# Kernel optimization log

Hardware: AMD Instinct MI355X
Metric: run time of the kernel (lower is better)

The kernel has to match this reference:

```python
import jax, jax.numpy as jnp
import numpy as np

R_SPHERE = 3.0   # bounding_sphere_radius
NEAR = 0.0       # near_distance
FAR = 100.0      # far_distance
SECANT_STEPS = 4 # manifold_secant_steps
EPS = 1e-4
R0 = 1.0         # base radius of analytic manifold field


def setup_inputs() -> dict:
    key = jax.random.key(0)
    ks = jax.random.split(key, 6)
    B, R, L, H = 4, 8192, 4, 64
    rays_o = jax.random.normal(ks[0], (B, R, 3), dtype=jnp.float32) * 0.2  # origins inside sphere
    rd = jax.random.normal(ks[1], (B, R, 3), dtype=jnp.float32)
    rays_d = rd / jnp.linalg.norm(rd, axis=-1, keepdims=True)
    levels = jnp.linspace(0.5, -0.5, L, dtype=jnp.float32)  # manifold_levels parameter
    W1 = jax.random.normal(ks[2], (3, H), dtype=jnp.float32) * 0.3
    b1 = jnp.zeros((H,), dtype=jnp.float32)
    W2 = jax.random.normal(ks[3], (H, 1), dtype=jnp.float32) * 0.1
    b2 = jnp.zeros((1,), dtype=jnp.float32)
    rays_idx = jax.random.randint(ks[4], (B, R), 0, B, dtype=jnp.int64) if jax.config.jax_enable_x64 else jax.random.randint(ks[4], (B, R), 0, B, dtype=jnp.int32)
    mask_gt = jnp.ones((B, R), dtype=bool)
    return {"rays_o": rays_o, "rays_d": rays_d, "levels": levels, "W1": W1, "b1": b1,
            "W2": W2, "b2": b2, "mask_gt": mask_gt, "rays_idx": rays_idx, "num_samples": 64}


def _ray_march(rays_o, rays_d, levels, W1, b1, W2, b2, num_samples):
    B, Rn = rays_o.shape[:2]
    N = B * Rn
    L = levels.shape[0]
    o = rays_o.reshape(N, 3)
    d = rays_d.reshape(N, 3)

    def manifold_fn(x):
        # analytic stand-in for M(x_d, idx): scalar field + validity mask
        h = jnp.tanh(x @ W1 + b1)
        nrm = jnp.linalg.norm(x, axis=-1)
        s = (h @ W2)[..., 0] + b2[0] + (R0 - nrm)
        return s, nrm < R_SPHERE

    # ray-sphere intersection (unit-norm directions assumed, as in source)
    b = jnp.sum(o * d, axis=-1)
    c = jnp.sum(o * o, axis=-1) - R_SPHERE ** 2
    disc = b * b - c
    hit = disc > 0
    sq = jnp.sqrt(jnp.where(hit, disc, 1.0))
    d_near = jnp.maximum(-b - sq, NEAR)
    d_far = jnp.minimum(-b + sq, FAR)
    mask_bound = hit & (d_near < d_far)

    # stratified (uniform) depth samples, (N, S)
    t = jnp.linspace(0.0, 1.0, num_samples, dtype=rays_o.dtype)[None, :]
    ds = d_near[:, None] * (1 - t) + d_far[:, None] * t
    x_d = o[:, None, :] + d[:, None, :] * ds[..., None]  # (N, S, 3)
    scal, m_valid = manifold_fn(x_d)                      # (N, S)

    # --- find_closest_interval ---
    S = num_samples
    dep_f, dep_b = ds[:, :-1], ds[:, 1:]
    sc_f, sc_b = scal[:, :-1], scal[:, 1:]
    m_pair = m_valid[:, :-1] & m_valid[:, 1:]
    l3 = levels[None, :, None]                            # (1, L, 1)
    in_interval = (sc_f[:, None, :] >= l3) & (l3 >= sc_b[:, None, :]) & m_pair[:, None, :]
    rank = jnp.sign(l3 - sc_b[:, None, :]) * jnp.arange(S - 1, 0, -1, dtype=scal.dtype)
    ind_closest = jnp.argmax(rank, axis=2)                # (N, L)
    ind_lowest = jnp.broadcast_to(jnp.argmin(sc_b, axis=1)[:, None], (N, L))
    mask_surface = jnp.any(in_interval, axis=2)
    idx = jnp.where(mask_surface, ind_closest, ind_lowest)
    d_front = jnp.take_along_axis(dep_f, idx, axis=1)
    d_back = jnp.take_along_axis(dep_b, idx, axis=1)
    s_front = jnp.take_along_axis(sc_f, idx, axis=1)
    s_back = jnp.take_along_axis(sc_b, idx, axis=1)

    # --- find_exact_intersection ---
    lr = levels[None, :]                                  # (1, L)
    s_diff = s_front - s_back
    m_vdiff = jnp.abs(s_diff) > EPS
    mask_intersect = (s_front >= lr) & (lr >= s_back)
    mask_secant = mask_intersect & m_vdiff
    s_diff_safe = jnp.where(m_vdiff, s_diff, 1.0)
    d_secant = ((lr - s_back) * d_front + (s_front - lr) * d_back) / s_diff_safe
    d_init = jnp.where(mask_secant, d_secant, d_back)

    # secant refinement (fixed step count; masked full-array updates replace
    # torch's boolean-indexed subset updates with identical math on masked lanes)
    dfs, dbs, sfs, sbs, dcur = d_front, d_back, s_front, s_back, d_init
    for _ in range(SECANT_STEPS):
        x_mid = o[:, None, :] + dcur[..., None] * d[:, None, :]  # (N, L, 3)
        s_mid, mv = manifold_fn(x_mid)
        upf = (s_mid > lr) & mv
        upb = (s_mid < lr) & mv
        dfs = jnp.where(upf, dcur, dfs)
        sfs = jnp.where(upf, s_mid, sfs)
        dbs = jnp.where(upb, dcur, dbs)
        sbs = jnp.where(upb, s_mid, sbs)
        sd = sfs - sbs
        ok = jnp.abs(sd) > EPS
        dcur = jnp.where(ok, ((lr - sbs) * dfs + (sfs - lr) * dbs) / jnp.where(ok, sd, 1.0), dcur)
    d_intersect = jnp.where(mask_secant, dcur, d_init)

    # sort intersections by depth (use_presort=False branch)
    order = jnp.argsort(d_intersect, axis=1)
    d_intersect = jnp.take_along_axis(d_intersect, order, axis=1)
    mask_intersect = jnp.take_along_axis(mask_intersect, order, axis=1)

    dist = jnp.where(mask_bound[:, None], d_intersect, 0.0).reshape(B, Rn, L)
    mask = (mask_intersect & mask_bound[:, None]).reshape(B, Rn, L)
    return dist, mask


def reference(rays_o, rays_d, levels, W1, b1, W2, b2, mask_gt, rays_idx, num_samples):
    # mask_gt / rays_idx are unused in eval mode (use_gt_mask_when_training=False,
    # analytic manifold_fn ignores batch index), kept for signature fidelity.
    return _ray_march(rays_o, rays_d, levels, W1, b1, W2, b2, num_samples)
```

## Files before the change

kernel.cpp:

```cpp
#include <hip/hip_runtime.h>
#include <cstdint>

#define R_SPHEREf 3.0f
#define NEARf 0.0f
#define FARf 100.0f
#define SECANT_STEPS 4
#define EPSf 1e-4f
#define R0f 1.0f
#define Hh 64
#define Lc 4
#define Sn 64

#define C_HI 2.88539004325866699f
#define C_LO 3.8519227871e-08f

__global__ __launch_bounds__(256) void manifold_render_kernel(
    const float* __restrict__ rays_o, const float* __restrict__ rays_d,
    const float* __restrict__ levels, const float* __restrict__ W1,
    const float* __restrict__ b1, const float* __restrict__ W2,
    const float* __restrict__ b2, float* __restrict__ out, int N)
{
    __shared__ float4 abq[4][Hh];

    const int tid = threadIdx.x;
    const int wave = tid >> 6;
    const int lane = tid & 63;
    const int r = blockIdx.x * 4 + wave;
    const bool ray_ok = (r < N);

    const float b2v = b2[0];
    float lvl[Lc];
#pragma unroll
    for (int j = 0; j < Lc; ++j) lvl[j] = levels[j];

    float ox = 0.f, oy = 0.f, oz = 0.f, dx = 0.f, dy = 0.f, dz = 1.f;
    if (ray_ok) {
        ox = rays_o[3 * r]; oy = rays_o[3 * r + 1]; oz = rays_o[3 * r + 2];
        dx = rays_d[3 * r]; dy = rays_d[3 * r + 1]; dz = rays_d[3 * r + 2];
    }

    float w2lane;
    {
        const float w1x = W1[lane], w1y = W1[Hh + lane], w1z = W1[2 * Hh + lane];
        w2lane = W2[lane];
        const float Ah = __builtin_fmaf(oz, w1z, __builtin_fmaf(oy, w1y,
                         __builtin_fmaf(ox, w1x, b1[lane])));
        const float Bh = __builtin_fmaf(dz, w1z, __builtin_fmaf(dy, w1y, dx * w1x));
        const float A2 = __builtin_fmaf(Ah, C_LO, Ah * C_HI);
        const float B2 = __builtin_fmaf(Bh, C_LO, Bh * C_HI);
        abq[wave][lane] = make_float4(A2, B2, -2.0f * w2lane, 0.0f);
    }
    float w2sum = w2lane;
#pragma unroll
    for (int m = 1; m < 64; m <<= 1) w2sum += __shfl_xor(w2sum, m);
    const float sbase = w2sum + b2v + R0f;

    __syncthreads();
    if (!ray_ok) return;

    const float bq = ox * dx + oy * dy + oz * dz;
    const float cq = ox * ox + oy * oy + oz * oz - R_SPHEREf * R_SPHEREf;
    const float disc = bq * bq - cq;
    const bool hit = disc > 0.0f;
    const float sq = sqrtf(hit ? disc : 1.0f);
    const float d_near = fmaxf(-bq - sq, NEARf);
    const float d_far  = fminf(-bq + sq, FARf);
    const bool mask_bound = hit && (d_near < d_far);

    const float t = (float)lane / (float)(Sn - 1);
    const float dsv = d_near * (1.0f - t) + d_far * t;
    const float x0 = ox + dx * dsv, x1 = oy + dy * dsv, x2 = oz + dz * dsv;
    const float nrm = sqrtf(x0 * x0 + x1 * x1 + x2 * x2);

    const float4* __restrict__ ab = &abq[wave][0];
    float acc = 0.0f;
#pragma unroll
    for (int h = 0; h < Hh; ++h) {
        const float4 q = ab[h];
        const float y = __builtin_fmaf(dsv, q.y, q.x);
        const float e = __builtin_amdgcn_exp2f(y);
        const float r1 = __builtin_amdgcn_rcpf(e + 1.0f);
        acc = __builtin_fmaf(q.z, r1, acc);
    }
    const float scal = (acc + sbase) - nrm;
    const bool valid = nrm < R_SPHEREf;

    const float scb = __shfl_down(scal, 1);
    const int validn = __shfl_down((int)valid, 1);
    const bool is_int = lane < (Sn - 1);

    float keyv = is_int ? scb : INFINITY;
    int keyi = lane;
#pragma unroll
    for (int m = 1; m < 64; m <<= 1) {
        float ov = __shfl_xor(keyv, m);
        int oi = __shfl_xor(keyi, m);
        if (ov < keyv || (ov == keyv && oi < keyi)) { keyv = ov; keyi = oi; }
    }
    const int ind_lowest = keyi;

    const bool inint_base = is_int && valid && (validn != 0);

    bool mintb[Lc], msec[Lc];
    float dinit[Lc];
    float g_dfs = 0.f, g_dbs = 0.f, g_sfs = 0.f, g_sbs = 0.f, g_dcur = 0.f, g_lr = 0.f;
    const int g = lane >> 4;

#pragma unroll
    for (int lv = 0; lv < Lc; ++lv) {
        const float l = lvl[lv];
        unsigned long long bP = __ballot(is_int && (scb < l));
        unsigned long long bZ = __ballot(is_int && (scb == l));
        unsigned long long bI = __ballot(inint_base && (scal >= l) && (l >= scb));
        int ind_closest = bP ? __builtin_ctzll(bP)
                             : (bZ ? __builtin_ctzll(bZ) : (Sn - 2));
        bool mask_surface = (bI != 0ULL);
        int idx = mask_surface ? ind_closest : ind_lowest;

        float d_front = __shfl(dsv, idx);
        float d_back  = __shfl(dsv, idx + 1);
        float s_front = __shfl(scal, idx);
        float s_back  = __shfl(scal, idx + 1);

        bool mi = (s_front >= l) && (l >= s_back);
        float sd = s_front - s_back;
        bool vd = fabsf(sd) > EPSf;
        bool ms = mi && vd;
        float d_sec = ((l - s_back) * d_front + (s_front - l) * d_back) / (vd ? sd : 1.0f);
        float di = ms ? d_sec : d_back;

        mintb[lv] = mi; msec[lv] = ms; dinit[lv] = di;
        if (g == lv) {
            g_dfs = d_front; g_dbs = d_back; g_sfs = s_front; g_sbs = s_back;
            g_dcur = di; g_lr = l;
        }
    }

    const int sub = lane & 15;
    float4 sq0 = ab[sub], sq1 = ab[sub + 16], sq2 = ab[sub + 32], sq3 = ab[sub + 48];

#pragma unroll
    for (int it = 0; it < SECANT_STEPS; ++it) {
        float mx0 = ox + g_dcur * dx, mx1 = oy + g_dcur * dy, mx2 = oz + g_dcur * dz;
        float mn = sqrtf(mx0 * mx0 + mx1 * mx1 + mx2 * mx2);
        float part;
        {
            float y0 = __builtin_fmaf(g_dcur, sq0.y, sq0.x);
            float y1 = __builtin_fmaf(g_dcur, sq1.y, sq1.x);
            float y2 = __builtin_fmaf(g_dcur, sq2.y, sq2.x);
            float y3 = __builtin_fmaf(g_dcur, sq3.y, sq3.x);
            float r0 = __builtin_amdgcn_rcpf(__builtin_amdgcn_exp2f(y0) + 1.0f);
            float r1 = __builtin_amdgcn_rcpf(__builtin_amdgcn_exp2f(y1) + 1.0f);
            float r2 = __builtin_amdgcn_rcpf(__builtin_amdgcn_exp2f(y2) + 1.0f);
            float r3 = __builtin_amdgcn_rcpf(__builtin_amdgcn_exp2f(y3) + 1.0f);
            part = sq0.z * r0;
            part = __builtin_fmaf(sq1.z, r1, part);
            part = __builtin_fmaf(sq2.z, r2, part);
            part = __builtin_fmaf(sq3.z, r3, part);
        }
#pragma unroll
        for (int m = 1; m < 16; m <<= 1) part += __shfl_xor(part, m, 16);
        float s_mid = (part + sbase) - mn;
        bool mv = mn < R_SPHEREf;
        bool upf = (s_mid > g_lr) && mv;
        bool upb = (s_mid < g_lr) && mv;
        if (upf) { g_dfs = g_dcur; g_sfs = s_mid; }
        if (upb) { g_dbs = g_dcur; g_sbs = s_mid; }
        float sd2 = g_sfs - g_sbs;
        bool ok = fabsf(sd2) > EPSf;
        if (ok) g_dcur = ((g_lr - g_sbs) * g_dfs + (g_sfs - g_lr) * g_dbs) / sd2;
    }

    float v0, v1, v2, v3;
    {
        float dc0 = __shfl(g_dcur, 0);
        float dc1 = __shfl(g_dcur, 16);
        float dc2 = __shfl(g_dcur, 32);
        float dc3 = __shfl(g_dcur, 48);
        v0 = msec[0] ? dc0 : dinit[0];
        v1 = msec[1] ? dc1 : dinit[1];
        v2 = msec[2] ? dc2 : dinit[2];
        v3 = msec[3] ? dc3 : dinit[3];
    }
    int m0 = mintb[0], m1 = mintb[1], m2 = mintb[2], m3 = mintb[3];
    int i0 = 0, i1 = 1, i2 = 2, i3 = 3;

#define CSWAP(va, ia, ma, vb, ib, mb)                                    \
    { bool sw = (vb < va) || (vb == va && ib < ia);                      \
      if (sw) { float tv = va; va = vb; vb = tv;                         \
                int ti = ia; ia = ib; ib = ti;                           \
                int tm = ma; ma = mb; mb = tm; } }
    CSWAP(v0, i0, m0, v1, i1, m1);
    CSWAP(v2, i2, m2, v3, i3, m3);
    CSWAP(v0, i0, m0, v2, i2, m2);
    CSWAP(v1, i1, m1, v3, i3, m3);
    CSWAP(v1, i1, m1, v2, i2, m2);
#undef CSWAP

    const long long NL = (long long)N * Lc;
    if (lane < Lc) {
        float dv = (lane == 0) ? v0 : (lane == 1) ? v1 : (lane == 2) ? v2 : v3;
        out[(long long)r * Lc + lane] = mask_bound ? dv : 0.0f;
    } else if (lane < 2 * Lc) {
        int k = lane - Lc;
        int mm = (k == 0) ? m0 : (k == 1) ? m1 : (k == 2) ? m2 : m3;
        out[NL + (long long)r * Lc + k] = (mm && mask_bound) ? 1.0f : 0.0f;
    }
}

extern "C" void kernel_launch(void* const* d_in, const int* in_sizes, int n_in,
                              void* d_out, int out_size, void* d_ws, size_t ws_size,
                              hipStream_t stream) {
    const float* rays_o = (const float*)d_in[0];
    const float* rays_d = (const float*)d_in[1];
    const float* levels = (const float*)d_in[2];
    const float* W1 = (const float*)d_in[3];
    const float* b1 = (const float*)d_in[4];
    const float* W2 = (const float*)d_in[5];
    const float* b2 = (const float*)d_in[6];
    float* out = (float*)d_out;

    const int N = in_sizes[0] / 3;
    const int blocks = (N + 3) / 4;
    manifold_render_kernel<<<blocks, 256, 0, stream>>>(
        rays_o, rays_d, levels, W1, b1, W2, b2, out, N);
}
```

Before: 130.3 us.

## Use DPP row rotations instead of LDS broadcasts and shuffles in MLP loop

The hidden-unit loop no longer reads each of the 64 coefficient float4s from LDS. Each lane loads four float4s and rotates them across its 16-lane row with DPP row_ror, so the whole row covers all units without LDS traffic. The first four butterfly steps of the argmin and the 16-lane secant reduction also switch from ds_swizzle/bpermute shuffles to DPP row rotations. This trades LDS reads for three extra VALU DPP moves per hidden unit and changes the summation order of the field values.

```diff
diff --git a/kernel.cpp b/kernel.cpp
--- a/kernel.cpp
+++ b/kernel.cpp
@@ -13,6 +13,24 @@
 
 #define C_HI 2.88539004325866699f
 #define C_LO 3.8519227871e-08f
+
+template <int CTRL>
+__device__ __forceinline__ float dpp_rot(float v) {
+    int i = __float_as_int(v);
+    int r = __builtin_amdgcn_update_dpp(i, i, CTRL, 0xF, 0xF, false);
+    return __int_as_float(r);
+}
+template <int CTRL>
+__device__ __forceinline__ int dpp_rot_i(int v) {
+    return __builtin_amdgcn_update_dpp(v, v, CTRL, 0xF, 0xF, false);
+}
+__device__ __forceinline__ float row16_sum(float x) {
+    x += dpp_rot<0x128>(x);
+    x += dpp_rot<0x124>(x);
+    x += dpp_rot<0x122>(x);
+    x += dpp_rot<0x121>(x);
+    return x;
+}
 
 __global__ __launch_bounds__(256) void manifold_render_kernel(
     const float* __restrict__ rays_o, const float* __restrict__ rays_d,
@@ -73,14 +91,29 @@
     const float nrm = sqrtf(x0 * x0 + x1 * x1 + x2 * x2);
 
     const float4* __restrict__ ab = &abq[wave][0];
+    const int Rrow = lane >> 4;
+    const int s16 = lane & 15;
+
+    float4 qq[4];
+#pragma unroll
+    for (int k = 0; k < 4; ++k) qq[k] = ab[(((Rrow + k) & 3) << 4) + s16];
+
     float acc = 0.0f;
 #pragma unroll
-    for (int h = 0; h < Hh; ++h) {
-        const float4 q = ab[h];
-        const float y = __builtin_fmaf(dsv, q.y, q.x);
-        const float e = __builtin_amdgcn_exp2f(y);
-        const float r1 = __builtin_amdgcn_rcpf(e + 1.0f);
-        acc = __builtin_fmaf(q.z, r1, acc);
+    for (int k = 0; k < 4; ++k) {
+        float cA = qq[k].x, cB = qq[k].y, cW = qq[k].z;
+#pragma unroll
+        for (int i = 0; i < 16; ++i) {
+            const float y = __builtin_fmaf(dsv, cB, cA);
+            const float e = __builtin_amdgcn_exp2f(y);
+            const float r1 = __builtin_amdgcn_rcpf(e + 1.0f);
+            acc = __builtin_fmaf(cW, r1, acc);
+            if (i < 15) {
+                cA = dpp_rot<0x121>(cA);
+                cB = dpp_rot<0x121>(cB);
+                cW = dpp_rot<0x121>(cW);
+            }
+        }
     }
     const float scal = (acc + sbase) - nrm;
     const bool valid = nrm < R_SPHEREf;
@@ -91,8 +124,16 @@
 
     float keyv = is_int ? scb : INFINITY;
     int keyi = lane;
-#pragma unroll
-    for (int m = 1; m < 64; m <<= 1) {
+#define ARGMIN_STEP_DPP(CTRL)                                            \
+    { float ov = dpp_rot<CTRL>(keyv); int oi = dpp_rot_i<CTRL>(keyi);    \
+      if (ov < keyv || (ov == keyv && oi < keyi)) { keyv = ov; keyi = oi; } }
+    ARGMIN_STEP_DPP(0x128)
+    ARGMIN_STEP_DPP(0x124)
+    ARGMIN_STEP_DPP(0x122)
+    ARGMIN_STEP_DPP(0x121)
+#undef ARGMIN_STEP_DPP
+#pragma unroll
+    for (int m = 16; m < 64; m <<= 1) {
         float ov = __shfl_xor(keyv, m);
         int oi = __shfl_xor(keyi, m);
         if (ov < keyv || (ov == keyv && oi < keyi)) { keyv = ov; keyi = oi; }
@@ -158,8 +199,7 @@
             part = __builtin_fmaf(sq2.z, r2, part);
             part = __builtin_fmaf(sq3.z, r3, part);
         }
-#pragma unroll
-        for (int m = 1; m < 16; m <<= 1) part += __shfl_xor(part, m, 16);
+        part = row16_sum(part);
         float s_mid = (part + sbase) - mn;
         bool mv = mn < R_SPHEREf;
         bool upf = (s_mid > g_lr) && mv;
```

Result: slower. 143.5 us (+10.1%).

## Transpose MLP sample loop: per-hidden-unit geometric exp recurrence with butterfly reduction

Applied to the files above, without the earlier changes.

Each lane now owns one hidden unit and evaluates it at all 64 uniform samples. The exponential is computed once per group of 8 samples and stepped forward by multiplying with a constant ratio. The reciprocal comes from a bit-trick seed refined by three Newton iterations instead of the hardware rcp. A 6-stage shuffle transpose-reduction then gives each lane the sum for its own sample, replacing 64 LDS reads plus exp and rcp per lane. The change trades transcendental instructions for more FMAs, a large register array (p[64]) and many cross-lane shuffles, which may raise register pressure, lower occupancy, and add rounding drift from the repeated multiplication.

```diff
diff --git a/kernel.cpp b/kernel.cpp
--- a/kernel.cpp
+++ b/kernel.cpp
@@ -14,6 +14,14 @@
 #define C_HI 2.88539004325866699f
 #define C_LO 3.8519227871e-08f
 
+__device__ __forceinline__ float rcp_fr(float den) {
+    float g = __int_as_float(0x7EF311C3 - __float_as_int(den));
+    g = g * __builtin_fmaf(-den, g, 2.0f);
+    g = g * __builtin_fmaf(-den, g, 2.0f);
+    g = g * __builtin_fmaf(-den, g, 2.0f);
+    return g;
+}
+
 __global__ __launch_bounds__(256) void manifold_render_kernel(
     const float* __restrict__ rays_o, const float* __restrict__ rays_d,
     const float* __restrict__ levels, const float* __restrict__ W1,
@@ -39,23 +47,24 @@
         dx = rays_d[3 * r]; dy = rays_d[3 * r + 1]; dz = rays_d[3 * r + 2];
     }
 
-    float w2lane;
+    float A2, B2, m2w2;
     {
         const float w1x = W1[lane], w1y = W1[Hh + lane], w1z = W1[2 * Hh + lane];
-        w2lane = W2[lane];
+        const float w2lane = W2[lane];
         const float Ah = __builtin_fmaf(oz, w1z, __builtin_fmaf(oy, w1y,
                          __builtin_fmaf(ox, w1x, b1[lane])));
         const float Bh = __builtin_fmaf(dz, w1z, __builtin_fmaf(dy, w1y, dx * w1x));
-        const float A2 = __builtin_fmaf(Ah, C_LO, Ah * C_HI);
-        const float B2 = __builtin_fmaf(Bh, C_LO, Bh * C_HI);
-        abq[wave][lane] = make_float4(A2, B2, -2.0f * w2lane, 0.0f);
-    }
-    float w2sum = w2lane;
-#pragma unroll
-    for (int m = 1; m < 64; m <<= 1) w2sum += __shfl_xor(w2sum, m);
-    const float sbase = w2sum + b2v + R0f;
-
+        A2 = __builtin_fmaf(Ah, C_LO, Ah * C_HI);
+        B2 = __builtin_fmaf(Bh, C_LO, Bh * C_HI);
+        m2w2 = -2.0f * w2lane;
+        abq[wave][lane] = make_float4(A2, B2, m2w2, 0.0f);
+        float w2sum = w2lane;
+#pragma unroll
+        for (int m = 1; m < 64; m <<= 1) w2sum += __shfl_xor(w2sum, m);
+        abq[wave][lane].w = w2sum;
+    }
     __syncthreads();
+    const float sbase = abq[wave][0].w + b2v + R0f;
     if (!ray_ok) return;
 
     const float bq = ox * dx + oy * dy + oz * dz;
@@ -67,22 +76,38 @@
     const float d_far  = fminf(-bq + sq, FARf);
     const bool mask_bound = hit && (d_near < d_far);
 
+    const float dt = (d_far - d_near) * (1.0f / 63.0f);
+    const float rho = __builtin_amdgcn_exp2f(B2 * dt);
+    float p[Sn];
+#pragma unroll
+    for (int b = 0; b < 8; ++b) {
+        const float t0 = __builtin_fmaf((float)(8 * b), dt, d_near);
+        float E = __builtin_amdgcn_exp2f(__builtin_fmaf(t0, B2, A2));
+#pragma unroll
+        for (int j = 0; j < 8; ++j) {
+            p[8 * b + j] = m2w2 * rcp_fr(E + 1.0f);
+            if (j < 7) E *= rho;
+        }
+    }
+#pragma unroll
+    for (int b = 5; b >= 0; --b) {
+        const int m = 1 << b;
+        const bool hb = (lane & m) != 0;
+#pragma unroll
+        for (int j = 0; j < m; ++j) {
+            const float a = p[j], c = p[j + m];
+            const float send = hb ? a : c;
+            const float recv = __shfl_xor(send, m);
+            const float keep = hb ? c : a;
+            p[j] = keep + recv;
+        }
+    }
+
     const float t = (float)lane / (float)(Sn - 1);
     const float dsv = d_near * (1.0f - t) + d_far * t;
     const float x0 = ox + dx * dsv, x1 = oy + dy * dsv, x2 = oz + dz * dsv;
     const float nrm = sqrtf(x0 * x0 + x1 * x1 + x2 * x2);
-
-    const float4* __restrict__ ab = &abq[wave][0];
-    float acc = 0.0f;
-#pragma unroll
-    for (int h = 0; h < Hh; ++h) {
-        const float4 q = ab[h];
-        const float y = __builtin_fmaf(dsv, q.y, q.x);
-        const float e = __builtin_amdgcn_exp2f(y);
-        const float r1 = __builtin_amdgcn_rcpf(e + 1.0f);
-        acc = __builtin_fmaf(q.z, r1, acc);
-    }
-    const float scal = (acc + sbase) - nrm;
+    const float scal = (p[0] + sbase) - nrm;
     const bool valid = nrm < R_SPHEREf;
 
     const float scb = __shfl_down(scal, 1);
@@ -136,6 +161,7 @@
         }
     }
 
+    const float4* __restrict__ ab = &abq[wave][0];
     const int sub = lane & 15;
     float4 sq0 = ab[sub], sq1 = ab[sub + 16], sq2 = ab[sub + 32], sq3 = ab[sub + 48];
 
```

New measurement: 135.2 us. 3.8% more time.
